# Kernel optimization log

Measured on AMD Instinct MI355X. Metric: run time of the kernel, lower is better.

Reference implementation:

```python
import jax, jax.numpy as jnp
import numpy as np

B, N_SRC, N_TGT = 2, 2048, 2048
DIM, HEADS, DIM_HEAD, DIM_ROT = 1024, 16, 64, 32
INNER = HEADS * DIM_HEAD
SCALE = DIM_HEAD ** -0.5


def rotate_every_two(x):
    # (..., d) with d even: pairs (x1, x2) -> (-x2, x1), interleaved
    x1 = x[..., ::2]
    x2 = x[..., 1::2]
    return jnp.stack((-x2, x1), axis=-1).reshape(x.shape)


def setup_inputs() -> dict:
    key = jax.random.key(0)
    ks = jax.random.split(key, 10)
    return {
        "src": jax.random.normal(ks[0], (B, N_SRC, DIM), jnp.float32),
        "sin_src": jax.random.uniform(ks[1], (B, N_SRC, DIM_ROT), jnp.float32, -1.0, 1.0),
        "cos_src": jax.random.uniform(ks[2], (B, N_SRC, DIM_ROT), jnp.float32, -1.0, 1.0),
        "tgt": jax.random.normal(ks[3], (B, N_TGT, DIM), jnp.float32),
        "sin_tgt": jax.random.uniform(ks[4], (B, N_TGT, DIM_ROT), jnp.float32, -1.0, 1.0),
        "cos_tgt": jax.random.uniform(ks[5], (B, N_TGT, DIM_ROT), jnp.float32, -1.0, 1.0),
        "wq": jax.random.normal(ks[6], (DIM, INNER), jnp.float32) / np.sqrt(DIM),
        "wkv": jax.random.normal(ks[7], (DIM, 2 * INNER), jnp.float32) / np.sqrt(DIM),
        "wout": jax.random.normal(ks[8], (INNER, DIM), jnp.float32) / np.sqrt(INNER),
        "bout": jnp.zeros((DIM,), jnp.float32),
    }


def reference(src, sin_src, cos_src, tgt, sin_tgt, cos_tgt, wq, wkv, wout, bout):
    b = src.shape[0]
    q = tgt @ wq                                  # (b, i, inner)
    k, v = jnp.split(src @ wkv, 2, axis=-1)       # (b, j, inner) each

    def split_heads(t):
        return t.reshape(b, t.shape[1], HEADS, DIM_HEAD).transpose(0, 2, 1, 3)

    q, k, v = map(split_heads, (q, k, v))          # (b, h, n, d)

    # rotary on leading DIM_ROT dims; pos embs broadcast across heads
    st, ct = sin_tgt[:, None], cos_tgt[:, None]    # (b, 1, i, dr)
    ss, cs = sin_src[:, None], cos_src[:, None]    # (b, 1, j, dr)
    q_rot, q_pass = q[..., :DIM_ROT], q[..., DIM_ROT:]
    k_rot, k_pass = k[..., :DIM_ROT], k[..., DIM_ROT:]
    q_rot = q_rot * ct + rotate_every_two(q_rot) * st
    k_rot = k_rot * cs + rotate_every_two(k_rot) * ss
    q = jnp.concatenate([q_rot, q_pass], axis=-1)
    k = jnp.concatenate([k_rot, k_pass], axis=-1)

    dots = jnp.einsum('bhid,bhjd->bhij', q, k) * SCALE
    attn = jax.nn.softmax(dots, axis=-1)
    out = jnp.einsum('bhij,bhjd->bhid', attn, v)
    out = out.transpose(0, 2, 1, 3).reshape(b, out.shape[2], INNER)
    return out @ wout + bout, attn
```

## Files before the change

### kernel.cpp

```cpp
#include <hip/hip_runtime.h>
#include <hip/hip_bf16.h>
#include <cstdint>
#include <cstddef>

#define NB 2
#define NSEQ 2048
#define NHEADS 16
#define HD 64
#define DMODEL 1024
#define SCALEF 0.125f

typedef __attribute__((ext_vector_type(4))) float f32x4;
typedef __attribute__((ext_vector_type(8))) short s16x8;

__device__ __forceinline__ unsigned short f2bf(float f) {
  union { float f; unsigned u; } v; v.f = f;
  unsigned u = v.u;
  return (unsigned short)((u + 0x7fffu + ((u >> 16) & 1u)) >> 16);
}
__device__ __forceinline__ float bf2f(unsigned short s) {
  union { unsigned u; float f; } v; v.u = ((unsigned)s) << 16;
  return v.f;
}

__global__ void k_convert2(const float* __restrict__ a, const float* __restrict__ b,
                           unsigned short* __restrict__ oa, unsigned short* __restrict__ ob) {
  int bx = blockIdx.x;
  const float* in = (bx < 4096) ? a : b;
  unsigned short* out = (bx < 4096) ? oa : ob;
  int i = (bx & 4095) * 256 + threadIdx.x;
  float4 v = ((const float4*)in)[i];
  ushort4 o;
  o.x = f2bf(v.x); o.y = f2bf(v.y); o.z = f2bf(v.z); o.w = f2bf(v.w);
  ((ushort4*)out)[i] = o;
}

__global__ void k_transpose_all(const float* __restrict__ wq, unsigned short* __restrict__ wq_t,
                                const float* __restrict__ wkv, unsigned short* __restrict__ wkv_t,
                                const float* __restrict__ wout, unsigned short* __restrict__ wout_t) {
  const int z = blockIdx.z;
  const float* w; unsigned short* wt; int N;
  if (z == 0)      { w = wq;   wt = wq_t;   N = 1024; }
  else if (z == 1) { w = wkv;  wt = wkv_t;  N = 2048; }
  else             { w = wout; wt = wout_t; N = 1024; }
  if (blockIdx.x * 64 >= N) return;
  __shared__ float t[64][65];
  int n0 = blockIdx.x * 64, k0 = blockIdx.y * 64;
  int c = threadIdx.x & 63, rb = threadIdx.x >> 6;
#pragma unroll
  for (int rr = 0; rr < 16; rr++) {
    int k = rb * 16 + rr;
    t[c][k] = w[(size_t)(k0 + k) * N + n0 + c];
  }
  __syncthreads();
#pragma unroll
  for (int rr = 0; rr < 16; rr++) {
    int n = rb * 16 + rr;
    wt[(size_t)(n0 + n) * 1024 + k0 + c] = f2bf(t[n][c]);
  }
}

#define GLD16(gp, lp) __builtin_amdgcn_global_load_lds( \
    (const __attribute__((address_space(1))) unsigned int*)(gp), \
    (__attribute__((address_space(3))) unsigned int*)(lp), 16, 0, 0)

#define GEMM_BODY(A, Bt, NBLK)                                                  \
  __shared__ unsigned short As[128 * 32];                                       \
  __shared__ unsigned short Bs[128 * 32];                                       \
  const int tid = threadIdx.x;                                                  \
  const int lane = tid & 63, wid = tid >> 6;                                    \
  const int m0 = blockIdx.y * 128, n0 = (NBLK) * 128;                           \
  const int wr = wid >> 1, wc = wid & 1;                                        \
  const int lr = lane >> 2, l4 = lane & 3;                                      \
  const int lc = lane & 15, lg = lane >> 4;                                     \
  const unsigned short* pa0 = (A) + (size_t)(m0 + wid * 32 + lr) * 1024 + l4 * 8; \
  const unsigned short* pa1 = pa0 + (size_t)16 * 1024;                          \
  const unsigned short* pb0 = (Bt) + (size_t)(n0 + wid * 32 + lr) * 1024 + l4 * 8;\
  const unsigned short* pb1 = pb0 + (size_t)16 * 1024;                          \
  f32x4 acc[4][4] = {};                                                         \
  for (int kt = 0; kt < 1024; kt += 32) {                                       \
    GLD16(pa0 + kt, &As[wid * 1024]);                                           \
    GLD16(pa1 + kt, &As[wid * 1024 + 512]);                                     \
    GLD16(pb0 + kt, &Bs[wid * 1024]);                                           \
    GLD16(pb1 + kt, &Bs[wid * 1024 + 512]);                                     \
    __syncthreads();                                                            \
    s16x8 af[4], bfr[4];                                                        \
    _Pragma("unroll")                                                           \
    for (int m = 0; m < 4; m++)                                                 \
      af[m] = *(const s16x8*)&As[(wr * 64 + m * 16 + lc) * 32 + lg * 8];        \
    _Pragma("unroll")                                                           \
    for (int n = 0; n < 4; n++)                                                 \
      bfr[n] = *(const s16x8*)&Bs[(wc * 64 + n * 16 + lc) * 32 + lg * 8];       \
    __builtin_amdgcn_s_setprio(1);                                              \
    _Pragma("unroll")                                                           \
    for (int m = 0; m < 4; m++)                                                 \
      _Pragma("unroll")                                                         \
      for (int n = 0; n < 4; n++)                                               \
        acc[m][n] = __builtin_amdgcn_mfma_f32_16x16x32_bf16(af[m], bfr[n], acc[m][n], 0, 0, 0); \
    __builtin_amdgcn_s_setprio(0);                                              \
    __syncthreads();                                                            \
  }

__global__ __launch_bounds__(256) void k_gemm(const unsigned short* __restrict__ A,
                                              const unsigned short* __restrict__ Bt,
                                              float* __restrict__ C,
                                              const float* __restrict__ bias) {
  GEMM_BODY(A, Bt, blockIdx.x)
  float bv[4];
#pragma unroll
  for (int n = 0; n < 4; n++) bv[n] = bias[n0 + wc * 64 + n * 16 + lc];
#pragma unroll
  for (int m = 0; m < 4; m++) {
#pragma unroll
    for (int n = 0; n < 4; n++) {
      int col = n0 + wc * 64 + n * 16 + lc;
#pragma unroll
      for (int r = 0; r < 4; r++) {
        int row = m0 + wr * 64 + m * 16 + lg * 4 + r;
        C[(size_t)row * 1024 + col] = acc[m][n][r] + bv[n];
      }
    }
  }
}

__global__ __launch_bounds__(256) void k_gemmqkv(const unsigned short* __restrict__ tgtb,
                                                 const unsigned short* __restrict__ srcb,
                                                 const unsigned short* __restrict__ wqt,
                                                 const unsigned short* __restrict__ wkvt,
                                                 const float* __restrict__ sin_t,
                                                 const float* __restrict__ cos_t,
                                                 const float* __restrict__ sin_s,
                                                 const float* __restrict__ cos_s,
                                                 unsigned short* __restrict__ qhb,
                                                 unsigned short* __restrict__ khb,
                                                 unsigned short* __restrict__ vtb) {
  const bool isq = (blockIdx.x < 8);
  const unsigned short* A  = isq ? tgtb : srcb;
  const unsigned short* Bt = isq ? wqt : wkvt;
  const float* sinp = isq ? sin_t : sin_s;
  const float* cosp = isq ? cos_t : cos_s;
  GEMM_BODY(A, Bt, (isq ? blockIdx.x : blockIdx.x - 8))
  if (isq) {
#pragma unroll
    for (int m = 0; m < 4; m++) {
#pragma unroll
      for (int n = 0; n < 4; n++) {
        int c = n0 + wc * 64 + n * 16 + lc;
        int h = c >> 6, d = c & 63;
        bool dorope = (d < 32);
#pragma unroll
        for (int r = 0; r < 4; r++) {
          int row = m0 + wr * 64 + m * 16 + lg * 4 + r;
          float x = acc[m][n][r];
          float px = __shfl_xor(x, 1);
          float o = x;
          if (dorope) {
            float s = sinp[(size_t)row * 32 + d];
            float cz = cosp[(size_t)row * 32 + d];
            o = (d & 1) ? (x * cz + px * s) : (x * cz - px * s);
          }
          int b = row >> 11, i = row & 2047;
          qhb[((size_t)(b * NHEADS + h) * NSEQ + i) * HD + d] = f2bf(o);
        }
      }
    }
  } else {
#pragma unroll
    for (int m = 0; m < 4; m++) {
#pragma unroll
      for (int n = 0; n < 4; n++) {
        int c = n0 + wc * 64 + n * 16 + lc;
        int d = c & 63;
        if (c < 1024) {
          int h = c >> 6;
          bool dorope = (d < 32);
#pragma unroll
          for (int r = 0; r < 4; r++) {
            int row = m0 + wr * 64 + m * 16 + lg * 4 + r;
            float x = acc[m][n][r];
            float px = __shfl_xor(x, 1);
            float o = x;
            if (dorope) {
              float s = sinp[(size_t)row * 32 + d];
              float cz = cosp[(size_t)row * 32 + d];
              o = (d & 1) ? (x * cz + px * s) : (x * cz - px * s);
            }
            int b = row >> 11, i = row & 2047;
            khb[((size_t)(b * NHEADS + h) * NSEQ + i) * HD + d] = f2bf(o);
          }
        } else {
          int h = (c - 1024) >> 6;
#pragma unroll
          for (int r = 0; r < 4; r++) (void)__shfl_xor(acc[m][n][r], 1);
          ushort4 o;
          o.x = f2bf(acc[m][n][0]); o.y = f2bf(acc[m][n][1]);
          o.z = f2bf(acc[m][n][2]); o.w = f2bf(acc[m][n][3]);
          int row0 = m0 + wr * 64 + m * 16 + lg * 4;
          int b = row0 >> 11, i = row0 & 2047;
          *(ushort4*)&vtb[((size_t)(b * NHEADS + h) * HD + d) * NSEQ + i] = o;
        }
      }
    }
  }
}

#define QBLK 32
#define SROWB 2056
__global__ __launch_bounds__(1024, 4) void k_attn(const unsigned short* __restrict__ qh,
                                                  const unsigned short* __restrict__ kh,
                                                  const unsigned short* __restrict__ vt,
                                                  float* __restrict__ attn_g,
                                                  unsigned short* __restrict__ ctx) {
  __shared__ unsigned short Sbf[QBLK * SROWB];
  __shared__ float wred[16][32];
  __shared__ float invr[32];
  float* part = (float*)Sbf;

  const int tid = threadIdx.x;
  const int lane = tid & 63, wid = tid >> 6;
  const int bid = blockIdx.x;
  const int g = bid & 31, t = bid >> 5;
  const int h = g & 15, b = g >> 4;
  const int i0 = t * QBLK;
  const int lc = lane & 15, lg = lane >> 4;
  const int wcb = wid * 128;

  const unsigned short* qb = qh + ((size_t)(b * NHEADS + h) * NSEQ + i0) * HD;
  const unsigned short* kb = kh + (size_t)(b * NHEADS + h) * NSEQ * HD;
  const unsigned short* vb = vt + (size_t)(b * NHEADS + h) * HD * NSEQ;

  s16x8 aq[2][2];
#pragma unroll
  for (int rg = 0; rg < 2; rg++) {
    aq[rg][0] = *(const s16x8*)&qb[(rg * 16 + lc) * HD + lg * 8];
    aq[rg][1] = *(const s16x8*)&qb[(rg * 16 + lc) * HD + 32 + lg * 8];
  }
  float psum[2][4] = {};
  const unsigned short* krow = kb + (size_t)(wcb + lc) * HD + lg * 8;
  s16x8 kp[2][2];
  kp[0][0] = *(const s16x8*)&krow[0];
  kp[0][1] = *(const s16x8*)&krow[32];
#pragma unroll
  for (int jf = 0; jf < 8; jf++) {
    if (jf < 7) {
      kp[(jf + 1) & 1][0] = *(const s16x8*)&krow[(size_t)((jf + 1) * 16) * HD];
      kp[(jf + 1) & 1][1] = *(const s16x8*)&krow[(size_t)((jf + 1) * 16) * HD + 32];
    }
    int j = wcb + jf * 16;
#pragma unroll
    for (int rg = 0; rg < 2; rg++) {
      f32x4 acc = {};
      acc = __builtin_amdgcn_mfma_f32_16x16x32_bf16(aq[rg][0], kp[jf & 1][0], acc, 0, 0, 0);
      acc = __builtin_amdgcn_mfma_f32_16x16x32_bf16(aq[rg][1], kp[jf & 1][1], acc, 0, 0, 0);
#pragma unroll
      for (int r = 0; r < 4; r++) {
        float e = __expf(acc[r] * SCALEF);
        psum[rg][r] += e;
        Sbf[(size_t)(rg * 16 + lg * 4 + r) * SROWB + j + lc] = f2bf(e);
      }
    }
  }
#pragma unroll
  for (int off = 1; off <= 8; off <<= 1)
#pragma unroll
    for (int rg = 0; rg < 2; rg++)
#pragma unroll
      for (int r = 0; r < 4; r++) psum[rg][r] += __shfl_xor(psum[rg][r], off);
  if (lc == 0) {
#pragma unroll
    for (int rg = 0; rg < 2; rg++)
#pragma unroll
      for (int r = 0; r < 4; r++) wred[wid][rg * 16 + lg * 4 + r] = psum[rg][r];
  }
  __syncthreads();
  if (tid < 32) {
    float tot = 0.f;
#pragma unroll
    for (int w = 0; w < 16; w++) tot += wred[w][tid];
    invr[tid] = 1.0f / tot;
  }
  __syncthreads();

  const int srow = tid >> 5;
  const int scc = (tid & 31) * 8;
  const float sinv = invr[srow];
  float* arow = attn_g + ((size_t)(b * NHEADS + h) * NSEQ + i0 + srow) * NSEQ + scc;

  f32x4 accd[2][4] = {};
  const unsigned short* vrow = vb + (size_t)lc * NSEQ + wcb + lg * 8;
  s16x8 vp[2][4];
#pragma unroll
  for (int f = 0; f < 4; f++)
    vp[0][f] = *(const s16x8*)&vrow[(size_t)(f * 16) * NSEQ];
#pragma unroll
  for (int jj = 0; jj < 4; jj++) {
    if (jj < 3) {
#pragma unroll
      for (int f = 0; f < 4; f++)
        vp[(jj + 1) & 1][f] = *(const s16x8*)&vrow[(size_t)(f * 16) * NSEQ + (jj + 1) * 32];
    }
    int jb = wcb + jj * 32;
    s16x8 af0 = *(const s16x8*)&Sbf[(size_t)lc * SROWB + jb + lg * 8];
    __builtin_amdgcn_s_setprio(1);
#pragma unroll
    for (int f = 0; f < 4; f++)
      accd[0][f] = __builtin_amdgcn_mfma_f32_16x16x32_bf16(af0, vp[jj & 1][f], accd[0][f], 0, 0, 0);
    __builtin_amdgcn_s_setprio(0);
    s16x8 af1 = *(const s16x8*)&Sbf[(size_t)(16 + lc) * SROWB + jb + lg * 8];
    __builtin_amdgcn_s_setprio(1);
#pragma unroll
    for (int f = 0; f < 4; f++)
      accd[1][f] = __builtin_amdgcn_mfma_f32_16x16x32_bf16(af1, vp[jj & 1][f], accd[1][f], 0, 0, 0);
    __builtin_amdgcn_s_setprio(0);
#pragma unroll
    for (int kk = 0; kk < 2; kk++) {
      int k = jj * 2 + kk;
      s16x8 ev = *(const s16x8*)&Sbf[(size_t)srow * SROWB + scc + k * 256];
      f32x4 f0, f1;
      f0[0] = bf2f((unsigned short)ev[0]) * sinv;
      f0[1] = bf2f((unsigned short)ev[1]) * sinv;
      f0[2] = bf2f((unsigned short)ev[2]) * sinv;
      f0[3] = bf2f((unsigned short)ev[3]) * sinv;
      f1[0] = bf2f((unsigned short)ev[4]) * sinv;
      f1[1] = bf2f((unsigned short)ev[5]) * sinv;
      f1[2] = bf2f((unsigned short)ev[6]) * sinv;
      f1[3] = bf2f((unsigned short)ev[7]) * sinv;
      *(f32x4*)&arow[k * 256] = f0;
      *(f32x4*)&arow[k * 256 + 4] = f1;
    }
  }
  __syncthreads();

  if (wid < 8) {
#pragma unroll
    for (int rg = 0; rg < 2; rg++)
#pragma unroll
      for (int f = 0; f < 4; f++)
#pragma unroll
        for (int r = 0; r < 4; r++)
          part[((size_t)wid * 32 + rg * 16 + lg * 4 + r) * 65 + f * 16 + lc] = accd[rg][f][r];
  }
  __syncthreads();
  if (wid >= 8) {
#pragma unroll
    for (int rg = 0; rg < 2; rg++)
#pragma unroll
      for (int f = 0; f < 4; f++)
#pragma unroll
        for (int r = 0; r < 4; r++)
          part[((size_t)(wid - 8) * 32 + rg * 16 + lg * 4 + r) * 65 + f * 16 + lc] += accd[rg][f][r];
  }
  __syncthreads();

  {
    const int oi = tid >> 5;
    const int d0 = (tid & 31) * 2;
    float s0 = 0.f, s1 = 0.f;
#pragma unroll
    for (int p = 0; p < 8; p++) {
      s0 += part[((size_t)p * 32 + oi) * 65 + d0];
      s1 += part[((size_t)p * 32 + oi) * 65 + d0 + 1];
    }
    float iv = invr[oi];
    ushort2 o;
    o.x = f2bf(s0 * iv);
    o.y = f2bf(s1 * iv);
    *(ushort2*)&ctx[(size_t)(b * NSEQ + i0 + oi) * DMODEL + h * HD + d0] = o;
  }
}

extern "C" void kernel_launch(void* const* d_in, const int* in_sizes, int n_in,
                              void* d_out, int out_size, void* d_ws, size_t ws_size,
                              hipStream_t stream) {
  const float* src     = (const float*)d_in[0];
  const float* sin_src = (const float*)d_in[1];
  const float* cos_src = (const float*)d_in[2];
  const float* tgt     = (const float*)d_in[3];
  const float* sin_tgt = (const float*)d_in[4];
  const float* cos_tgt = (const float*)d_in[5];
  const float* wq      = (const float*)d_in[6];
  const float* wkv     = (const float*)d_in[7];
  const float* wout    = (const float*)d_in[8];
  const float* bout    = (const float*)d_in[9];

  if (ws_size < (size_t)109051904) return;

  uint8_t* w = (uint8_t*)d_ws;
  unsigned short* tgt_bf = (unsigned short*)(w + 0);
  unsigned short* src_bf = (unsigned short*)(w + 8388608);
  unsigned short* wq_t   = (unsigned short*)(w + 16777216);
  unsigned short* wkv_t  = (unsigned short*)(w + 18874368);
  unsigned short* wout_t = (unsigned short*)(w + 23068672);
  unsigned short* qhb    = (unsigned short*)(w + 75497472);
  unsigned short* khb    = (unsigned short*)(w + 83886080);
  unsigned short* vtb    = (unsigned short*)(w + 92274688);
  unsigned short* ctx    = (unsigned short*)(w + 100663296);

  float* out_p  = (float*)d_out;
  float* attn_p = out_p + (size_t)NB * NSEQ * DMODEL;

  k_convert2<<<8192, 256, 0, stream>>>(tgt, src, tgt_bf, src_bf);
  k_transpose_all<<<dim3(32, 16, 3), 256, 0, stream>>>(wq, wq_t, wkv, wkv_t, wout, wout_t);

  k_gemmqkv<<<dim3(24, 32), 256, 0, stream>>>(tgt_bf, src_bf, wq_t, wkv_t,
                                              sin_tgt, cos_tgt, sin_src, cos_src,
                                              qhb, khb, vtb);

  k_attn<<<2048, 1024, 0, stream>>>(qhb, khb, vtb, attn_p, ctx);

  k_gemm<<<dim3(8, 32), 256, 0, stream>>>(ctx, wout_t, out_p, bout);
}
```

Measured before the change: 332.6 us.

## Make attention blocks persistent over eight query tiles with deferred attn stores

The attention kernel now launches 256 blocks, and each block loops over eight consecutive 32-row query tiles instead of handling one tile per block. The normalized attn-row writes for one tile are stashed in registers and issued during the next tile's QK^T phase, so the fp32 attention-matrix stores overlap with MFMA work. This adds register pressure (stash[8]) and an extra barrier per iteration. With 256 blocks of 1024 threads there may be fewer resident waves than CUs can hold, which risks lower occupancy and load balance.

```diff
diff --git a/kernel.cpp b/kernel.cpp
--- a/kernel.cpp
+++ b/kernel.cpp
@@ -219,153 +219,177 @@
   const int tid = threadIdx.x;
   const int lane = tid & 63, wid = tid >> 6;
   const int bid = blockIdx.x;
-  const int g = bid & 31, t = bid >> 5;
+  const int g = bid & 31, sub = bid >> 5;
   const int h = g & 15, b = g >> 4;
-  const int i0 = t * QBLK;
   const int lc = lane & 15, lg = lane >> 4;
   const int wcb = wid * 128;
 
-  const unsigned short* qb = qh + ((size_t)(b * NHEADS + h) * NSEQ + i0) * HD;
   const unsigned short* kb = kh + (size_t)(b * NHEADS + h) * NSEQ * HD;
   const unsigned short* vb = vt + (size_t)(b * NHEADS + h) * HD * NSEQ;
-
-  s16x8 aq[2][2];
-#pragma unroll
-  for (int rg = 0; rg < 2; rg++) {
-    aq[rg][0] = *(const s16x8*)&qb[(rg * 16 + lc) * HD + lg * 8];
-    aq[rg][1] = *(const s16x8*)&qb[(rg * 16 + lc) * HD + 32 + lg * 8];
-  }
-  float psum[2][4] = {};
   const unsigned short* krow = kb + (size_t)(wcb + lc) * HD + lg * 8;
-  s16x8 kp[2][2];
-  kp[0][0] = *(const s16x8*)&krow[0];
-  kp[0][1] = *(const s16x8*)&krow[32];
-#pragma unroll
-  for (int jf = 0; jf < 8; jf++) {
-    if (jf < 7) {
-      kp[(jf + 1) & 1][0] = *(const s16x8*)&krow[(size_t)((jf + 1) * 16) * HD];
-      kp[(jf + 1) & 1][1] = *(const s16x8*)&krow[(size_t)((jf + 1) * 16) * HD + 32];
-    }
-    int j = wcb + jf * 16;
-#pragma unroll
-    for (int rg = 0; rg < 2; rg++) {
-      f32x4 acc = {};
-      acc = __builtin_amdgcn_mfma_f32_16x16x32_bf16(aq[rg][0], kp[jf & 1][0], acc, 0, 0, 0);
-      acc = __builtin_amdgcn_mfma_f32_16x16x32_bf16(aq[rg][1], kp[jf & 1][1], acc, 0, 0, 0);
-#pragma unroll
-      for (int r = 0; r < 4; r++) {
-        float e = __expf(acc[r] * SCALEF);
-        psum[rg][r] += e;
-        Sbf[(size_t)(rg * 16 + lg * 4 + r) * SROWB + j + lc] = f2bf(e);
-      }
-    }
-  }
-#pragma unroll
-  for (int off = 1; off <= 8; off <<= 1)
-#pragma unroll
-    for (int rg = 0; rg < 2; rg++)
-#pragma unroll
-      for (int r = 0; r < 4; r++) psum[rg][r] += __shfl_xor(psum[rg][r], off);
-  if (lc == 0) {
-#pragma unroll
-    for (int rg = 0; rg < 2; rg++)
-#pragma unroll
-      for (int r = 0; r < 4; r++) wred[wid][rg * 16 + lg * 4 + r] = psum[rg][r];
-  }
-  __syncthreads();
-  if (tid < 32) {
-    float tot = 0.f;
-#pragma unroll
-    for (int w = 0; w < 16; w++) tot += wred[w][tid];
-    invr[tid] = 1.0f / tot;
-  }
-  __syncthreads();
+  const unsigned short* vrow = vb + (size_t)lc * NSEQ + wcb + lg * 8;
 
   const int srow = tid >> 5;
   const int scc = (tid & 31) * 8;
-  const float sinv = invr[srow];
-  float* arow = attn_g + ((size_t)(b * NHEADS + h) * NSEQ + i0 + srow) * NSEQ + scc;
-
-  f32x4 accd[2][4] = {};
-  const unsigned short* vrow = vb + (size_t)lc * NSEQ + wcb + lg * 8;
-  s16x8 vp[2][4];
-#pragma unroll
-  for (int f = 0; f < 4; f++)
-    vp[0][f] = *(const s16x8*)&vrow[(size_t)(f * 16) * NSEQ];
-#pragma unroll
-  for (int jj = 0; jj < 4; jj++) {
-    if (jj < 3) {
+
+  s16x8 stash[8];
+  float sinv_prev = 0.f;
+  float* arow_prev = nullptr;
+
+  for (int it = 0; it < 8; it++) {
+    const int i0 = (sub * 8 + it) * QBLK;
+    const unsigned short* qb = qh + ((size_t)(b * NHEADS + h) * NSEQ + i0) * HD;
+
+    s16x8 aq[2][2];
+#pragma unroll
+    for (int rg = 0; rg < 2; rg++) {
+      aq[rg][0] = *(const s16x8*)&qb[(rg * 16 + lc) * HD + lg * 8];
+      aq[rg][1] = *(const s16x8*)&qb[(rg * 16 + lc) * HD + 32 + lg * 8];
+    }
+    float psum[2][4] = {};
+    s16x8 kp[2][2];
+    kp[0][0] = *(const s16x8*)&krow[0];
+    kp[0][1] = *(const s16x8*)&krow[32];
+#pragma unroll
+    for (int jf = 0; jf < 8; jf++) {
+      if (jf < 7) {
+        kp[(jf + 1) & 1][0] = *(const s16x8*)&krow[(size_t)((jf + 1) * 16) * HD];
+        kp[(jf + 1) & 1][1] = *(const s16x8*)&krow[(size_t)((jf + 1) * 16) * HD + 32];
+      }
+      if (it > 0) {
+        s16x8 ev = stash[jf];
+        f32x4 f0, f1;
+        f0[0] = bf2f((unsigned short)ev[0]) * sinv_prev;
+        f0[1] = bf2f((unsigned short)ev[1]) * sinv_prev;
+        f0[2] = bf2f((unsigned short)ev[2]) * sinv_prev;
+        f0[3] = bf2f((unsigned short)ev[3]) * sinv_prev;
+        f1[0] = bf2f((unsigned short)ev[4]) * sinv_prev;
+        f1[1] = bf2f((unsigned short)ev[5]) * sinv_prev;
+        f1[2] = bf2f((unsigned short)ev[6]) * sinv_prev;
+        f1[3] = bf2f((unsigned short)ev[7]) * sinv_prev;
+        *(f32x4*)&arow_prev[jf * 256] = f0;
+        *(f32x4*)&arow_prev[jf * 256 + 4] = f1;
+      }
+      int j = wcb + jf * 16;
+#pragma unroll
+      for (int rg = 0; rg < 2; rg++) {
+        f32x4 acc = {};
+        acc = __builtin_amdgcn_mfma_f32_16x16x32_bf16(aq[rg][0], kp[jf & 1][0], acc, 0, 0, 0);
+        acc = __builtin_amdgcn_mfma_f32_16x16x32_bf16(aq[rg][1], kp[jf & 1][1], acc, 0, 0, 0);
+#pragma unroll
+        for (int r = 0; r < 4; r++) {
+          float e = __expf(acc[r] * SCALEF);
+          psum[rg][r] += e;
+          Sbf[(size_t)(rg * 16 + lg * 4 + r) * SROWB + j + lc] = f2bf(e);
+        }
+      }
+    }
+#pragma unroll
+    for (int off = 1; off <= 8; off <<= 1)
+#pragma unroll
+      for (int rg = 0; rg < 2; rg++)
+#pragma unroll
+        for (int r = 0; r < 4; r++) psum[rg][r] += __shfl_xor(psum[rg][r], off);
+    if (lc == 0) {
+#pragma unroll
+      for (int rg = 0; rg < 2; rg++)
+#pragma unroll
+        for (int r = 0; r < 4; r++) wred[wid][rg * 16 + lg * 4 + r] = psum[rg][r];
+    }
+    __syncthreads();
+    if (tid < 32) {
+      float tot = 0.f;
+#pragma unroll
+      for (int w = 0; w < 16; w++) tot += wred[w][tid];
+      invr[tid] = 1.0f / tot;
+    }
+    __syncthreads();
+
+    f32x4 accd[2][4] = {};
+    s16x8 vp[2][4];
+#pragma unroll
+    for (int f = 0; f < 4; f++)
+      vp[0][f] = *(const s16x8*)&vrow[(size_t)(f * 16) * NSEQ];
+#pragma unroll
+    for (int jj = 0; jj < 4; jj++) {
+      if (jj < 3) {
+#pragma unroll
+        for (int f = 0; f < 4; f++)
+          vp[(jj + 1) & 1][f] = *(const s16x8*)&vrow[(size_t)(f * 16) * NSEQ + (jj + 1) * 32];
+      }
+      int jb = wcb + jj * 32;
+      s16x8 af0 = *(const s16x8*)&Sbf[(size_t)lc * SROWB + jb + lg * 8];
+      __builtin_amdgcn_s_setprio(1);
 #pragma unroll
       for (int f = 0; f < 4; f++)
-        vp[(jj + 1) & 1][f] = *(const s16x8*)&vrow[(size_t)(f * 16) * NSEQ + (jj + 1) * 32];
-    }
-    int jb = wcb + jj * 32;
-    s16x8 af0 = *(const s16x8*)&Sbf[(size_t)lc * SROWB + jb + lg * 8];
-    __builtin_amdgcn_s_setprio(1);
-#pragma unroll
-    for (int f = 0; f < 4; f++)
-      accd[0][f] = __builtin_amdgcn_mfma_f32_16x16x32_bf16(af0, vp[jj & 1][f], accd[0][f], 0, 0, 0);
-    __builtin_amdgcn_s_setprio(0);
-    s16x8 af1 = *(const s16x8*)&Sbf[(size_t)(16 + lc) * SROWB + jb + lg * 8];
-    __builtin_amdgcn_s_setprio(1);
-#pragma unroll
-    for (int f = 0; f < 4; f++)
-      accd[1][f] = __builtin_amdgcn_mfma_f32_16x16x32_bf16(af1, vp[jj & 1][f], accd[1][f], 0, 0, 0);
-    __builtin_amdgcn_s_setprio(0);
-#pragma unroll
-    for (int kk = 0; kk < 2; kk++) {
-      int k = jj * 2 + kk;
-      s16x8 ev = *(const s16x8*)&Sbf[(size_t)srow * SROWB + scc + k * 256];
-      f32x4 f0, f1;
-      f0[0] = bf2f((unsigned short)ev[0]) * sinv;
-      f0[1] = bf2f((unsigned short)ev[1]) * sinv;
-      f0[2] = bf2f((unsigned short)ev[2]) * sinv;
-      f0[3] = bf2f((unsigned short)ev[3]) * sinv;
-      f1[0] = bf2f((unsigned short)ev[4]) * sinv;
-      f1[1] = bf2f((unsigned short)ev[5]) * sinv;
-      f1[2] = bf2f((unsigned short)ev[6]) * sinv;
-      f1[3] = bf2f((unsigned short)ev[7]) * sinv;
-      *(f32x4*)&arow[k * 256] = f0;
-      *(f32x4*)&arow[k * 256 + 4] = f1;
-    }
-  }
-  __syncthreads();
-
-  if (wid < 8) {
-#pragma unroll
-    for (int rg = 0; rg < 2; rg++)
+        accd[0][f] = __builtin_amdgcn_mfma_f32_16x16x32_bf16(af0, vp[jj & 1][f], accd[0][f], 0, 0, 0);
+      __builtin_amdgcn_s_setprio(0);
+      s16x8 af1 = *(const s16x8*)&Sbf[(size_t)(16 + lc) * SROWB + jb + lg * 8];
+      __builtin_amdgcn_s_setprio(1);
 #pragma unroll
       for (int f = 0; f < 4; f++)
-#pragma unroll
-        for (int r = 0; r < 4; r++)
-          part[((size_t)wid * 32 + rg * 16 + lg * 4 + r) * 65 + f * 16 + lc] = accd[rg][f][r];
-  }
-  __syncthreads();
-  if (wid >= 8) {
-#pragma unroll
-    for (int rg = 0; rg < 2; rg++)
-#pragma unroll
-      for (int f = 0; f < 4; f++)
-#pragma unroll
-        for (int r = 0; r < 4; r++)
-          part[((size_t)(wid - 8) * 32 + rg * 16 + lg * 4 + r) * 65 + f * 16 + lc] += accd[rg][f][r];
-  }
-  __syncthreads();
-
-  {
-    const int oi = tid >> 5;
-    const int d0 = (tid & 31) * 2;
-    float s0 = 0.f, s1 = 0.f;
-#pragma unroll
-    for (int p = 0; p < 8; p++) {
-      s0 += part[((size_t)p * 32 + oi) * 65 + d0];
-      s1 += part[((size_t)p * 32 + oi) * 65 + d0 + 1];
-    }
-    float iv = invr[oi];
-    ushort2 o;
-    o.x = f2bf(s0 * iv);
-    o.y = f2bf(s1 * iv);
-    *(ushort2*)&ctx[(size_t)(b * NSEQ + i0 + oi) * DMODEL + h * HD + d0] = o;
+        accd[1][f] = __builtin_amdgcn_mfma_f32_16x16x32_bf16(af1, vp[jj & 1][f], accd[1][f], 0, 0, 0);
+      __builtin_amdgcn_s_setprio(0);
+      stash[jj * 2]     = *(const s16x8*)&Sbf[(size_t)srow * SROWB + scc + (jj * 2) * 256];
+      stash[jj * 2 + 1] = *(const s16x8*)&Sbf[(size_t)srow * SROWB + scc + (jj * 2 + 1) * 256];
+    }
+    sinv_prev = invr[srow];
+    arow_prev = attn_g + ((size_t)(b * NHEADS + h) * NSEQ + i0 + srow) * NSEQ + scc;
+    __syncthreads();
+
+    if (wid < 8) {
+#pragma unroll
+      for (int rg = 0; rg < 2; rg++)
+#pragma unroll
+        for (int f = 0; f < 4; f++)
+#pragma unroll
+          for (int r = 0; r < 4; r++)
+            part[((size_t)wid * 32 + rg * 16 + lg * 4 + r) * 65 + f * 16 + lc] = accd[rg][f][r];
+    }
+    __syncthreads();
+    if (wid >= 8) {
+#pragma unroll
+      for (int rg = 0; rg < 2; rg++)
+#pragma unroll
+        for (int f = 0; f < 4; f++)
+#pragma unroll
+          for (int r = 0; r < 4; r++)
+            part[((size_t)(wid - 8) * 32 + rg * 16 + lg * 4 + r) * 65 + f * 16 + lc] += accd[rg][f][r];
+    }
+    __syncthreads();
+
+    {
+      const int oi = tid >> 5;
+      const int d0 = (tid & 31) * 2;
+      float s0 = 0.f, s1 = 0.f;
+#pragma unroll
+      for (int p = 0; p < 8; p++) {
+        s0 += part[((size_t)p * 32 + oi) * 65 + d0];
+        s1 += part[((size_t)p * 32 + oi) * 65 + d0 + 1];
+      }
+      float iv = invr[oi];
+      ushort2 o;
+      o.x = f2bf(s0 * iv);
+      o.y = f2bf(s1 * iv);
+      *(ushort2*)&ctx[(size_t)(b * NSEQ + i0 + oi) * DMODEL + h * HD + d0] = o;
+    }
+    __syncthreads();
+  }
+
+#pragma unroll
+  for (int k = 0; k < 8; k++) {
+    s16x8 ev = stash[k];
+    f32x4 f0, f1;
+    f0[0] = bf2f((unsigned short)ev[0]) * sinv_prev;
+    f0[1] = bf2f((unsigned short)ev[1]) * sinv_prev;
+    f0[2] = bf2f((unsigned short)ev[2]) * sinv_prev;
+    f0[3] = bf2f((unsigned short)ev[3]) * sinv_prev;
+    f1[0] = bf2f((unsigned short)ev[4]) * sinv_prev;
+    f1[1] = bf2f((unsigned short)ev[5]) * sinv_prev;
+    f1[2] = bf2f((unsigned short)ev[6]) * sinv_prev;
+    f1[3] = bf2f((unsigned short)ev[7]) * sinv_prev;
+    *(f32x4*)&arow_prev[k * 256] = f0;
+    *(f32x4*)&arow_prev[k * 256 + 4] = f1;
   }
 }
 
@@ -406,7 +430,7 @@
                                               sin_tgt, cos_tgt, sin_src, cos_src,
                                               qhb, khb, vtb);
 
-  k_attn<<<2048, 1024, 0, stream>>>(qhb, khb, vtb, attn_p, ctx);
+  k_attn<<<256, 1024, 0, stream>>>(qhb, khb, vtb, attn_p, ctx);
 
   k_gemm<<<dim3(8, 32), 256, 0, stream>>>(ctx, wout_t, out_p, bout);
 }
```

Measured after the change: 494.0 us. 48.5% more time.
